# Optimization experiments

Hardware: AMD Instinct MI355X
Metric: run time of the kernel (lower is better)

Reference implementation:

```python
import jax, jax.numpy as jnp
import numpy as np

N, E, D, H, K = 100000, 1600000, 512, 256, 64


def setup_inputs() -> dict:
    key = jax.random.key(0)
    ks = jax.random.split(key, 8)
    x = jax.random.normal(ks[0], (N, D), dtype=jnp.float32)
    edge_index = jax.random.randint(ks[1], (2, E), 0, N, dtype=jnp.int64)
    W1 = jax.random.normal(ks[2], (D, H), dtype=jnp.float32) / np.sqrt(D)
    b1 = jnp.zeros((H,), dtype=jnp.float32)
    W2 = jax.random.normal(ks[3], (H, H), dtype=jnp.float32) / np.sqrt(H)
    b2 = jnp.zeros((H,), dtype=jnp.float32)
    Wk = jax.random.normal(ks[4], (H, K), dtype=jnp.float32) / np.sqrt(H)
    log_tau = jnp.array(np.log(1.0), dtype=jnp.float32)
    return {"x": x, "edge_index": edge_index, "W1": W1, "b1": b1,
            "W2": W2, "b2": b2, "Wk": Wk, "log_tau": log_tau}


def _gcn_norm(edge_index, n):
    # add self-loops, compute sym-normalized edge weights (PyG GCNConv default)
    loop = jnp.arange(n, dtype=edge_index.dtype)
    src = jnp.concatenate([edge_index[0], loop])
    dst = jnp.concatenate([edge_index[1], loop])
    deg = jax.ops.segment_sum(jnp.ones_like(dst, dtype=jnp.float32), dst, num_segments=n)
    dinv = jnp.where(deg > 0, jax.lax.rsqrt(deg), 0.0)
    norm = dinv[src] * dinv[dst]  # [E+N]
    return src, dst, norm


def _gcn_conv(h, W, b, src, dst, norm, n):
    hw = h @ W                      # dense GEMM [n, out]
    msg = hw[src] * norm[:, None]   # gather + scale
    out = jax.ops.segment_sum(msg, dst, num_segments=n)  # scatter-add
    return out + b


def reference(x, edge_index, W1, b1, W2, b2, Wk, log_tau):
    n = x.shape[0]
    src, dst, norm = _gcn_norm(edge_index, n)
    h = jax.nn.relu(_gcn_conv(x, W1, b1, src, dst, norm, n))
    h = _gcn_conv(h, W2, b2, src, dst, norm, n)
    logits = h @ Wk                 # [n, K]
    tau = jnp.exp(log_tau)
    S = jax.nn.softmax(logits / tau, axis=-1)
    return (S, logits)
```

## Files before the change

### kernel.cpp

```cpp
#include <hip/hip_runtime.h>

typedef unsigned short u16;
typedef unsigned int u32;

__device__ __forceinline__ float bfl(u32 u) { union { u32 i; float f; } v; v.i = u << 16; return v.f; }
__device__ __forceinline__ float bfh(u32 u) { union { u32 i; float f; } v; v.i = u & 0xffff0000u; return v.f; }
__device__ __forceinline__ float bf2f(u16 u) { union { u32 i; float f; } v; v.i = ((u32)u) << 16; return v.f; }
__device__ __forceinline__ u16 f2bf(float f) {
    union { float f; u32 i; } v; v.f = f;
    u32 r = v.i + 0x7fffu + ((v.i >> 16) & 1u);
    return (u16)(r >> 16);
}

typedef const __attribute__((address_space(1))) unsigned int* gas_u32;
typedef __attribute__((address_space(3))) unsigned int* las_u32;
__device__ __forceinline__ void async_cp16(const void* g, void* l) {
    __builtin_amdgcn_global_load_lds((gas_u32)g, (las_u32)l, 16, 0, 0);
}

__global__ void k_detect(const u32* __restrict__ xw, const int* __restrict__ eiw,
                         const void* __restrict__ ltau, int* __restrict__ flags,
                         int xwords, int E) {
    __shared__ int cf32, ci64nz;
    if (threadIdx.x == 0) { cf32 = 0; ci64nz = 0; }
    __syncthreads();
    int t = threadIdx.x;
    int xs = xwords / 256;
    u32 w = xw[(size_t)t * xs];
    int e = (int)((w >> 23) & 0xFFu);
    if (e >= 100 && e <= 140) atomicAdd(&cf32, 1);
    int es = E / 256;
    int hw = eiw[2 * (size_t)t * es + 1];
    if (hw != 0) atomicAdd(&ci64nz, 1);
    __syncthreads();
    if (t == 0) {
        int f32 = (cf32 >= 192) ? 1 : 0;
        flags[0] = f32;
        flags[1] = (ci64nz == 0) ? 1 : 0;
        ((float*)flags)[2] = f32 ? ((const float*)ltau)[0] : bf2f(((const u16*)ltau)[0]);
    }
}

__global__ void k_edges(const int* __restrict__ ei, int* __restrict__ src, int* __restrict__ dst,
                        int e, const int* __restrict__ flags) {
    int i = blockIdx.x * 256 + threadIdx.x;
    if (i >= e) return;
    if (flags[1]) { src[i] = ei[2 * i]; dst[i] = ei[2 * (e + i)]; }
    else          { src[i] = ei[i];     dst[i] = ei[e + i]; }
}

__global__ void k_deginit(int* deg, int n) {
    int i = blockIdx.x * 256 + threadIdx.x;
    if (i < n) deg[i] = 1;
}
__global__ void k_degcount(const int* __restrict__ dst, int* deg, int e) {
    int i = blockIdx.x * 256 + threadIdx.x;
    if (i < e) atomicAdd(&deg[dst[i]], 1);
}
__global__ void k_dinv(const int* __restrict__ deg, float* dinv, int n) {
    int i = blockIdx.x * 256 + threadIdx.x;
    if (i < n) dinv[i] = rsqrtf((float)deg[i]);
}
__global__ void k_blocksum(const int* __restrict__ deg, int* bsum, int n) {
    int b = blockIdx.x, t = threadIdx.x;
    int base = b * 1024 + t * 4;
    int s = 0;
#pragma unroll
    for (int j = 0; j < 4; j++) { int i = base + j; if (i < n) s += deg[i] - 1; }
    for (int d = 32; d; d >>= 1) s += __shfl_down(s, d);
    __shared__ int ws[4];
    int lane = t & 63, w = t >> 6;
    if (lane == 0) ws[w] = s;
    __syncthreads();
    if (t == 0) bsum[b] = ws[0] + ws[1] + ws[2] + ws[3];
}
__global__ void k_scanb(const int* __restrict__ bsum, int* boff, int nb, int* row_ptr, int n) {
    if (threadIdx.x == 0) {
        int acc = 0;
        for (int b = 0; b < nb; b++) { boff[b] = acc; acc += bsum[b]; }
        row_ptr[n] = acc;
    }
}
__global__ void k_scanwrite(const int* __restrict__ deg, const int* __restrict__ boff,
                            int* row_ptr, int* cursor, int n) {
    int b = blockIdx.x, t = threadIdx.x;
    int base = b * 1024 + t * 4;
    int v[4]; int s = 0;
#pragma unroll
    for (int j = 0; j < 4; j++) { int i = base + j; v[j] = (i < n) ? deg[i] - 1 : 0; s += v[j]; }
    int lane = t & 63, w = t >> 6;
    int inc = s;
    for (int d = 1; d < 64; d <<= 1) { int u = __shfl_up(inc, d); if (lane >= d) inc += u; }
    __shared__ int ws[4];
    if (lane == 63) ws[w] = inc;
    __syncthreads();
    int woff = 0;
    for (int i = 0; i < w; i++) woff += ws[i];
    int p = boff[b] + woff + inc - s;
#pragma unroll
    for (int j = 0; j < 4; j++) {
        int i = base + j;
        if (i < n) { row_ptr[i] = p; cursor[i] = p; p += v[j]; }
    }
}
__global__ void k_fill(const int* __restrict__ src, const int* __restrict__ dst,
                       int* cursor, int* col, int e) {
    int i = blockIdx.x * 256 + threadIdx.x;
    if (i < e) {
        int d = dst[i];
        int p = atomicAdd(&cursor[d], 1);
        col[p] = src[i];
    }
}
__global__ void k_transpose_flex(const void* __restrict__ in, u16* __restrict__ out,
                                 int R, int C, const int* __restrict__ flags) {
    int idx = blockIdx.x * 256 + threadIdx.x;
    if (idx >= R * C) return;
    u16 v = flags[0] ? f2bf(((const float*)in)[idx]) : ((const u16*)in)[idx];
    int r = idx / C, c = idx % C;
    out[(size_t)c * R + r] = v;
}

typedef __bf16 bf16x8 __attribute__((ext_vector_type(8)));
typedef float floatx4 __attribute__((ext_vector_type(4)));

template <int WROWS, int WCOLS, int TM, int TN, int MODE, bool AFLEX, bool OFLEX>
__global__ __launch_bounds__(256) void k_gemm_bt(const void* __restrict__ A,
                                                 const u16* __restrict__ Bt,
                                                 void* __restrict__ C,
                                                 const float* __restrict__ dinv,
                                                 const int* __restrict__ flags,
                                                 long long obase,
                                                 int M, int Nd, int Kd) {
    constexpr int BM = WROWS * TM * 16;
    constexpr int BN = WCOLS * TN * 16;
    constexpr int BK = 32;
    __shared__ u16 As[BM][BK];
    __shared__ u16 Bs[BN][BK];
    const int af32 = AFLEX ? flags[0] : 0;
    const int of32 = OFLEX ? flags[0] : 0;
    const int tid = threadIdx.x;
    const int m0 = blockIdx.y * BM;
    const int n0 = blockIdx.x * BN;
    const int lane = tid & 63;
    const int wave = tid >> 6;
    const int wm = wave / WCOLS;
    const int wn = wave % WCOLS;
    const int mrow = lane & 15;
    const int quad = lane >> 4;

    floatx4 acc[TM][TN];
#pragma unroll
    for (int i = 0; i < TM; i++)
#pragma unroll
        for (int j = 0; j < TN; j++) { floatx4 z = {0.f, 0.f, 0.f, 0.f}; acc[i][j] = z; }

    for (int kk = 0; kk < Kd; kk += BK) {
        if (AFLEX && af32) {
#pragma unroll
            for (int idx = tid * 8; idx < BM * BK; idx += 256 * 8) {
                int r = idx >> 5, k = idx & 31;
                int gr = m0 + r;
                u16 t8[8] = {0, 0, 0, 0, 0, 0, 0, 0};
                if (gr < M) {
                    const float* ap = (const float*)A + (size_t)gr * Kd + kk + k;
                    float4 f0 = *(const float4*)ap;
                    float4 f1 = *(const float4*)(ap + 4);
                    t8[0] = f2bf(f0.x); t8[1] = f2bf(f0.y); t8[2] = f2bf(f0.z); t8[3] = f2bf(f0.w);
                    t8[4] = f2bf(f1.x); t8[5] = f2bf(f1.y); t8[6] = f2bf(f1.z); t8[7] = f2bf(f1.w);
                }
                *(int4*)&As[r][k] = *(const int4*)t8;
            }
        } else {
#pragma unroll
            for (int idx = tid * 8; idx < BM * BK; idx += 256 * 8) {
                int r = idx >> 5, k = idx & 31;
                int gr = m0 + r;
                if (gr >= M) gr = M - 1;
                async_cp16((const u16*)A + (size_t)gr * Kd + kk + k, &As[r][k]);
            }
        }
#pragma unroll
        for (int idx = tid * 8; idx < BN * BK; idx += 256 * 8) {
            int r = idx >> 5, k = idx & 31;
            async_cp16(Bt + (size_t)(n0 + r) * Kd + kk + k, &Bs[r][k]);
        }
        __syncthreads();
        bf16x8 af[TM], bfr[TN];
#pragma unroll
        for (int i = 0; i < TM; i++)
            af[i] = *(const bf16x8*)&As[wm * TM * 16 + i * 16 + mrow][quad * 8];
#pragma unroll
        for (int j = 0; j < TN; j++)
            bfr[j] = *(const bf16x8*)&Bs[wn * TN * 16 + j * 16 + mrow][quad * 8];
#pragma unroll
        for (int i = 0; i < TM; i++)
#pragma unroll
            for (int j = 0; j < TN; j++)
                acc[i][j] = __builtin_amdgcn_mfma_f32_16x16x32_bf16(af[i], bfr[j], acc[i][j], 0, 0, 0);
        __syncthreads();
    }

#pragma unroll
    for (int i = 0; i < TM; i++) {
#pragma unroll
        for (int r = 0; r < 4; r++) {
            int grow = m0 + wm * TM * 16 + i * 16 + quad * 4 + r;
            if (grow < M) {
                float scale = (MODE == 0) ? dinv[grow] : 1.0f;
#pragma unroll
                for (int j = 0; j < TN; j++) {
                    int gcol = n0 + wn * TN * 16 + j * 16 + mrow;
                    float val = acc[i][j][r] * scale;
                    long long cidx = obase + (long long)grow * Nd + gcol;
                    if (OFLEX && of32) ((float*)C)[cidx] = val;
                    else               ((u16*)C)[cidx] = f2bf(val);
                }
            }
        }
    }
}

__global__ __launch_bounds__(256) void k_agg(const u16* __restrict__ g, u16* __restrict__ out,
                                             const int* __restrict__ row_ptr,
                                             const int* __restrict__ col,
                                             const float* __restrict__ dinv,
                                             const void* __restrict__ bias,
                                             const int* __restrict__ flags,
                                             int n, int do_relu) {
    int wid = (int)((blockIdx.x * 256 + threadIdx.x) >> 6);
    int lane = threadIdx.x & 63;
    if (wid >= n) return;
    const u16* gp = g + (size_t)lane * 4;
    uint2 rv = *(const uint2*)(gp + (size_t)wid * 256);
    float a0 = bfl(rv.x), a1 = bfh(rv.x), a2 = bfl(rv.y), a3 = bfh(rv.y);
    int beg = row_ptr[wid], end = row_ptr[wid + 1];
    for (int base = beg; base < end; base += 64) {
        int m = end - base; if (m > 64) m = 64;
        int ci = (base + lane < end) ? col[base + lane] : 0;
        int j = 0;
        for (; j + 4 <= m; j += 4) {
            int s0 = __shfl(ci, j);
            int s1 = __shfl(ci, j + 1);
            int s2 = __shfl(ci, j + 2);
            int s3 = __shfl(ci, j + 3);
            uint2 v0 = *(const uint2*)(gp + (size_t)s0 * 256);
            uint2 v1 = *(const uint2*)(gp + (size_t)s1 * 256);
            uint2 v2 = *(const uint2*)(gp + (size_t)s2 * 256);
            uint2 v3 = *(const uint2*)(gp + (size_t)s3 * 256);
            a0 += bfl(v0.x) + bfl(v1.x) + bfl(v2.x) + bfl(v3.x);
            a1 += bfh(v0.x) + bfh(v1.x) + bfh(v2.x) + bfh(v3.x);
            a2 += bfl(v0.y) + bfl(v1.y) + bfl(v2.y) + bfl(v3.y);
            a3 += bfh(v0.y) + bfh(v1.y) + bfh(v2.y) + bfh(v3.y);
        }
        for (; j < m; j++) {
            int s = __shfl(ci, j);
            uint2 v = *(const uint2*)(gp + (size_t)s * 256);
            a0 += bfl(v.x); a1 += bfh(v.x); a2 += bfl(v.y); a3 += bfh(v.y);
        }
    }
    float dv = dinv[wid];
    float b0, b1, b2, b3;
    if (flags[0]) {
        float4 q = ((const float4*)bias)[lane];
        b0 = q.x; b1 = q.y; b2 = q.z; b3 = q.w;
    } else {
        uint2 bv = ((const uint2*)bias)[lane];
        b0 = bfl(bv.x); b1 = bfh(bv.x); b2 = bfl(bv.y); b3 = bfh(bv.y);
    }
    a0 = a0 * dv + b0;
    a1 = a1 * dv + b1;
    a2 = a2 * dv + b2;
    a3 = a3 * dv + b3;
    if (do_relu) {
        a0 = fmaxf(a0, 0.f); a1 = fmaxf(a1, 0.f); a2 = fmaxf(a2, 0.f); a3 = fmaxf(a3, 0.f);
    }
    uint2 o;
    o.x = (u32)f2bf(a0) | ((u32)f2bf(a1) << 16);
    o.y = (u32)f2bf(a2) | ((u32)f2bf(a3) << 16);
    *(uint2*)(out + (size_t)wid * 256 + (size_t)lane * 4) = o;
}

__global__ __launch_bounds__(256) void k_softmax(void* __restrict__ out, long long NK,
                                                 const int* __restrict__ flags, int n) {
    int wid = (int)((blockIdx.x * 256 + threadIdx.x) >> 6);
    int lane = threadIdx.x & 63;
    if (wid >= n) return;
    int f32o = flags[0];
    float lt = ((const float*)flags)[2];
    float inv_tau = __expf(-lt);
    long long li = NK + (long long)wid * 64 + lane;
    float x = f32o ? ((const float*)out)[li] : bf2f(((const u16*)out)[li]);
    x *= inv_tau;
    float m = x;
    for (int d = 32; d; d >>= 1) m = fmaxf(m, __shfl_xor(m, d));
    float e = __expf(x - m);
    float s = e;
    for (int d = 32; d; d >>= 1) s += __shfl_xor(s, d);
    float r = e / s;
    long long si = (long long)wid * 64 + lane;
    if (f32o) ((float*)out)[si] = r;
    else      ((u16*)out)[si] = f2bf(r);
}

extern "C" void kernel_launch(void* const* d_in, const int* in_sizes, int n_in,
                              void* d_out, int out_size, void* d_ws, size_t ws_size,
                              hipStream_t stream) {
    const void* x    = d_in[0];
    const int*  ei   = (const int*)d_in[1];
    const void* W1   = d_in[2];
    const void* b1   = d_in[3];
    const void* W2   = d_in[4];
    const void* b2   = d_in[5];
    const void* Wk   = d_in[6];
    const void* ltau = d_in[7];
    const int D = 512, H = 256, K = 64;
    const int N = in_sizes[0] / D;
    const int E = in_sizes[1] / 2;
    const long long NK = (long long)N * K;

    u16* g = (u16*)d_ws;
    u16* h = g + (size_t)N * H;
    int* flags = (int*)(h + (size_t)N * H);
    int* srcv = (int*)g;
    int* dstv = srcv + E;

    size_t ooff = 0;
    auto oalloc = [&](size_t bytes) -> char* {
        char* p = (char*)d_out + ooff;
        ooff += (bytes + 255) & ~(size_t)255;
        return p;
    };
    int*   col     = (int*)oalloc((size_t)E * 4);
    int*   deg     = (int*)oalloc((size_t)N * 4);
    float* dinv    = (float*)oalloc((size_t)N * 4);
    int*   row_ptr = (int*)oalloc((size_t)(N + 1) * 4);
    int*   cursor  = (int*)oalloc((size_t)N * 4);
    int*   bsum    = (int*)oalloc(1024);
    int*   boff    = (int*)oalloc(1024);
    u16*   W1t     = (u16*)oalloc((size_t)D * H * 2);
    u16*   W2t     = (u16*)oalloc((size_t)H * H * 2);
    u16*   Wkt     = (u16*)oalloc((size_t)H * K * 2);

    const int nb = (N + 1023) / 1024;
    auto g256 = [](long long n) { return (int)((n + 255) / 256); };

    k_detect<<<1, 256, 0, stream>>>((const u32*)x, ei, ltau, flags, in_sizes[0] / 2, E);
    k_edges<<<g256(E), 256, 0, stream>>>(ei, srcv, dstv, E, flags);
    k_deginit<<<g256(N), 256, 0, stream>>>(deg, N);
    k_degcount<<<g256(E), 256, 0, stream>>>(dstv, deg, E);
    k_dinv<<<g256(N), 256, 0, stream>>>(deg, dinv, N);
    k_blocksum<<<nb, 256, 0, stream>>>(deg, bsum, N);
    k_scanb<<<1, 64, 0, stream>>>(bsum, boff, nb, row_ptr, N);
    k_scanwrite<<<nb, 256, 0, stream>>>(deg, boff, row_ptr, cursor, N);
    k_fill<<<g256(E), 256, 0, stream>>>(srcv, dstv, cursor, col, E);

    k_transpose_flex<<<g256((long long)D * H), 256, 0, stream>>>(W1, W1t, D, H, flags);
    k_transpose_flex<<<g256((long long)H * H), 256, 0, stream>>>(W2, W2t, H, H, flags);
    k_transpose_flex<<<g256((long long)H * K), 256, 0, stream>>>(Wk, Wkt, H, K, flags);

    const int mtiles = (N + 127) / 128;
    k_gemm_bt<2, 2, 4, 4, 0, true, false>
        <<<dim3(H / 128, mtiles), 256, 0, stream>>>(x, W1t, g, dinv, flags, 0, N, H, D);
    k_agg<<<g256((long long)N * 64), 256, 0, stream>>>(g, h, row_ptr, col, dinv, b1, flags, N, 1);
    k_gemm_bt<2, 2, 4, 4, 0, false, false>
        <<<dim3(H / 128, mtiles), 256, 0, stream>>>(h, W2t, g, dinv, flags, 0, N, H, H);
    k_agg<<<g256((long long)N * 64), 256, 0, stream>>>(g, h, row_ptr, col, dinv, b2, flags, N, 0);
    k_gemm_bt<4, 1, 2, 4, 1, false, true>
        <<<dim3(1, mtiles), 256, 0, stream>>>(h, Wkt, d_out, dinv, flags, NK, N, K, H);
    k_softmax<<<g256((long long)N * 64), 256, 0, stream>>>(d_out, NK, flags, N);
}
```

Before: 884.1 us.

## Double-buffer GEMM tiles, widen GEMM N-tile, and batch 8 gathers in aggregation

The GEMM kernel now double-buffers its A/B shared-memory tiles, issuing loads for the next K-step before computing the current one, and drops one barrier per iteration. The first two GEMMs use TN=8 so one block covers all 256 output columns, which avoids reading the A rows twice. The aggregation kernel issues 8 independent neighbour loads before accumulating, giving more memory-level parallelism. The trade-offs are double the LDS, higher register pressure from TN=8 accumulators under launch_bounds(256,2), and fewer GEMM blocks.

```diff
diff --git a/kernel.cpp b/kernel.cpp
--- a/kernel.cpp
+++ b/kernel.cpp
@@ -125,18 +125,18 @@
 typedef float floatx4 __attribute__((ext_vector_type(4)));
 
 template <int WROWS, int WCOLS, int TM, int TN, int MODE, bool AFLEX, bool OFLEX>
-__global__ __launch_bounds__(256) void k_gemm_bt(const void* __restrict__ A,
-                                                 const u16* __restrict__ Bt,
-                                                 void* __restrict__ C,
-                                                 const float* __restrict__ dinv,
-                                                 const int* __restrict__ flags,
-                                                 long long obase,
-                                                 int M, int Nd, int Kd) {
+__global__ __launch_bounds__(256, 2) void k_gemm_bt(const void* __restrict__ A,
+                                                    const u16* __restrict__ Bt,
+                                                    void* __restrict__ C,
+                                                    const float* __restrict__ dinv,
+                                                    const int* __restrict__ flags,
+                                                    long long obase,
+                                                    int M, int Nd, int Kd) {
     constexpr int BM = WROWS * TM * 16;
     constexpr int BN = WCOLS * TN * 16;
     constexpr int BK = 32;
-    __shared__ u16 As[BM][BK];
-    __shared__ u16 Bs[BN][BK];
+    __shared__ u16 As[2][BM][BK];
+    __shared__ u16 Bs[2][BN][BK];
     const int af32 = AFLEX ? flags[0] : 0;
     const int of32 = OFLEX ? flags[0] : 0;
     const int tid = threadIdx.x;
@@ -155,7 +155,7 @@
 #pragma unroll
         for (int j = 0; j < TN; j++) { floatx4 z = {0.f, 0.f, 0.f, 0.f}; acc[i][j] = z; }
 
-    for (int kk = 0; kk < Kd; kk += BK) {
+    auto stage = [&](int kk, int buf) {
         if (AFLEX && af32) {
 #pragma unroll
             for (int idx = tid * 8; idx < BM * BK; idx += 256 * 8) {
@@ -169,7 +169,13 @@
                     t8[0] = f2bf(f0.x); t8[1] = f2bf(f0.y); t8[2] = f2bf(f0.z); t8[3] = f2bf(f0.w);
                     t8[4] = f2bf(f1.x); t8[5] = f2bf(f1.y); t8[6] = f2bf(f1.z); t8[7] = f2bf(f1.w);
                 }
-                *(int4*)&As[r][k] = *(const int4*)t8;
+                *(int4*)&As[buf][r][k] = *(const int4*)t8;
+            }
+#pragma unroll
+            for (int idx = tid * 8; idx < BN * BK; idx += 256 * 8) {
+                int r = idx >> 5, k = idx & 31;
+                int4 v = *(const int4*)(Bt + (size_t)(n0 + r) * Kd + kk + k);
+                *(int4*)&Bs[buf][r][k] = v;
             }
         } else {
 #pragma unroll
@@ -177,28 +183,34 @@
                 int r = idx >> 5, k = idx & 31;
                 int gr = m0 + r;
                 if (gr >= M) gr = M - 1;
-                async_cp16((const u16*)A + (size_t)gr * Kd + kk + k, &As[r][k]);
+                async_cp16((const u16*)A + (size_t)gr * Kd + kk + k, &As[buf][r][k]);
+            }
+#pragma unroll
+            for (int idx = tid * 8; idx < BN * BK; idx += 256 * 8) {
+                int r = idx >> 5, k = idx & 31;
+                async_cp16(Bt + (size_t)(n0 + r) * Kd + kk + k, &Bs[buf][r][k]);
             }
         }
-#pragma unroll
-        for (int idx = tid * 8; idx < BN * BK; idx += 256 * 8) {
-            int r = idx >> 5, k = idx & 31;
-            async_cp16(Bt + (size_t)(n0 + r) * Kd + kk + k, &Bs[r][k]);
-        }
+    };
+
+    const int steps = Kd / BK;
+    stage(0, 0);
+    for (int s = 0; s < steps; s++) {
         __syncthreads();
+        if (s + 1 < steps) stage((s + 1) * BK, (s + 1) & 1);
+        const int b = s & 1;
         bf16x8 af[TM], bfr[TN];
 #pragma unroll
         for (int i = 0; i < TM; i++)
-            af[i] = *(const bf16x8*)&As[wm * TM * 16 + i * 16 + mrow][quad * 8];
+            af[i] = *(const bf16x8*)&As[b][wm * TM * 16 + i * 16 + mrow][quad * 8];
 #pragma unroll
         for (int j = 0; j < TN; j++)
-            bfr[j] = *(const bf16x8*)&Bs[wn * TN * 16 + j * 16 + mrow][quad * 8];
+            bfr[j] = *(const bf16x8*)&Bs[b][wn * TN * 16 + j * 16 + mrow][quad * 8];
 #pragma unroll
         for (int i = 0; i < TM; i++)
 #pragma unroll
             for (int j = 0; j < TN; j++)
                 acc[i][j] = __builtin_amdgcn_mfma_f32_16x16x32_bf16(af[i], bfr[j], acc[i][j], 0, 0, 0);
-        __syncthreads();
     }
 
 #pragma unroll
@@ -239,19 +251,18 @@
         int m = end - base; if (m > 64) m = 64;
         int ci = (base + lane < end) ? col[base + lane] : 0;
         int j = 0;
-        for (; j + 4 <= m; j += 4) {
-            int s0 = __shfl(ci, j);
-            int s1 = __shfl(ci, j + 1);
-            int s2 = __shfl(ci, j + 2);
-            int s3 = __shfl(ci, j + 3);
-            uint2 v0 = *(const uint2*)(gp + (size_t)s0 * 256);
-            uint2 v1 = *(const uint2*)(gp + (size_t)s1 * 256);
-            uint2 v2 = *(const uint2*)(gp + (size_t)s2 * 256);
-            uint2 v3 = *(const uint2*)(gp + (size_t)s3 * 256);
-            a0 += bfl(v0.x) + bfl(v1.x) + bfl(v2.x) + bfl(v3.x);
-            a1 += bfh(v0.x) + bfh(v1.x) + bfh(v2.x) + bfh(v3.x);
-            a2 += bfl(v0.y) + bfl(v1.y) + bfl(v2.y) + bfl(v3.y);
-            a3 += bfh(v0.y) + bfh(v1.y) + bfh(v2.y) + bfh(v3.y);
+        for (; j + 8 <= m; j += 8) {
+            uint2 v[8];
+#pragma unroll
+            for (int q = 0; q < 8; q++) {
+                int s = __shfl(ci, j + q);
+                v[q] = *(const uint2*)(gp + (size_t)s * 256);
+            }
+#pragma unroll
+            for (int q = 0; q < 8; q++) {
+                a0 += bfl(v[q].x); a1 += bfh(v[q].x);
+                a2 += bfl(v[q].y); a3 += bfh(v[q].y);
+            }
         }
         for (; j < m; j++) {
             int s = __shfl(ci, j);
@@ -360,11 +371,11 @@
     k_transpose_flex<<<g256((long long)H * K), 256, 0, stream>>>(Wk, Wkt, H, K, flags);
 
     const int mtiles = (N + 127) / 128;
-    k_gemm_bt<2, 2, 4, 4, 0, true, false>
-        <<<dim3(H / 128, mtiles), 256, 0, stream>>>(x, W1t, g, dinv, flags, 0, N, H, D);
+    k_gemm_bt<2, 2, 4, 8, 0, true, false>
+        <<<dim3(1, mtiles), 256, 0, stream>>>(x, W1t, g, dinv, flags, 0, N, H, D);
     k_agg<<<g256((long long)N * 64), 256, 0, stream>>>(g, h, row_ptr, col, dinv, b1, flags, N, 1);
-    k_gemm_bt<2, 2, 4, 4, 0, false, false>
-        <<<dim3(H / 128, mtiles), 256, 0, stream>>>(h, W2t, g, dinv, flags, 0, N, H, H);
+    k_gemm_bt<2, 2, 4, 8, 0, false, false>
+        <<<dim3(1, mtiles), 256, 0, stream>>>(h, W2t, g, dinv, flags, 0, N, H, H);
     k_agg<<<g256((long long)N * 64), 256, 0, stream>>>(g, h, row_ptr, col, dinv, b2, flags, N, 0);
     k_gemm_bt<4, 1, 2, 4, 1, false, true>
         <<<dim3(1, mtiles), 256, 0, stream>>>(h, Wkt, d_out, dinv, flags, NK, N, K, H);
```

New measurement: 870.4 us. About the same (-1.6%).
